# Kernel optimization log

Measured on AMD Instinct MI355X. Metric: run time of the kernel, lower is better.

The kernel has to match this reference:

```python
import jax, jax.numpy as jnp
import numpy as np

B, D, H, T = 8192, 256, 512, 4  # batch, latent dim, hidden units, num IAF transforms


def _made_masks():
    deg_in = np.arange(1, D + 1)                      # input degrees 1..D
    deg_h = 1 + (np.arange(H) % (D - 1))              # hidden degrees in [1, D-1]
    m1 = (deg_h[None, :] >= deg_in[:, None]).astype(np.float32)   # [D, H]
    m2 = (deg_h[None, :] >= deg_h[:, None]).astype(np.float32)    # [H, H]
    mo = (deg_in[None, :] > deg_h[:, None]).astype(np.float32)    # [H, D] strict for outputs
    m3 = np.repeat(mo, 2, axis=1)                     # [H, 2D]: params=2 per dim, interleaved
    return jnp.asarray(m1), jnp.asarray(m2), jnp.asarray(m3)

M1, M2, M3 = _made_masks()


def _made(x, w1, b1, w2, b2, w3, b3):
    h = jax.nn.relu(x @ (w1 * M1) + b1)
    h = jax.nn.relu(h @ (w2 * M2) + b2)
    out = (h @ (w3 * M3) + b3).reshape(x.shape[0], D, 2)
    shift, log_var = out[..., 0], out[..., 1]
    # lstm_flag == False branch of Made.call
    return shift, jnp.tanh(log_var)


def setup_inputs() -> dict:
    key = jax.random.key(0)
    ks = jax.random.split(key, 6)
    s1 = 0.05
    return {
        "mean": jax.random.normal(ks[0], (B, D), jnp.float32),
        "log_var": jax.random.normal(ks[1], (B, D), jnp.float32) * 0.5,
        "eps": jax.random.normal(ks[2], (B, D), jnp.float32),
        "W1": jax.random.normal(ks[3], (T, D, H), jnp.float32) * s1,
        "b1": jnp.zeros((T, H), jnp.float32),
        "W2": jax.random.normal(ks[4], (T, H, H), jnp.float32) * s1,
        "b2": jnp.zeros((T, H), jnp.float32),
        "W3": jax.random.normal(ks[5], (T, H, 2 * D), jnp.float32) * s1,
        "b3": jnp.zeros((T, 2 * D), jnp.float32),
    }


def reference(mean, log_var, eps, W1, b1, W2, b2, W3, b3):
    # Base sample from MultivariateNormalDiag(mean, exp(0.5*log_var))
    x = mean + jnp.exp(0.5 * log_var) * eps
    # Chain([IAF_0, Perm, IAF_1, Perm, ..., IAF_{T-1}, Perm]).forward applies the
    # LAST bijector first: Perm, then Invert(MAF)_{T-1}, ..., down to IAF_0.
    # Invert(MAF).forward == MAF.inverse: a single parallel MADE pass.
    for i in reversed(range(T)):
        x = x[..., ::-1]  # Permute(reversed(range(D)))
        shift, log_scale = _made(x, W1[i], b1[i], W2[i], b2[i], W3[i], b3[i])
        x = (x - shift) * jnp.exp(-log_scale)
    return x
```

## Files before the change

kernel.cpp:

```cpp
#include <hip/hip_runtime.h>


typedef _Float16 f16;
typedef __attribute__((ext_vector_type(8))) _Float16 f16x8;
typedef __attribute__((ext_vector_type(4))) float f32x4;

#define NB 8192
#define ND 256
#define NH 512
#define NT 4
#define XSTR 260

#define W1F_OFF 0
#define W2F_OFF (NT*NH*ND)
#define W3F_OFF (W2F_OFF + NT*NH*NH)
#define WS_ELEMS (W3F_OFF + NT*NH*NH)

__device__ __forceinline__ int h_orig(int j) {
  if (j < 3) return j == 0 ? 0 : (j == 1 ? 255 : 510);
  if (j < 6) return j == 3 ? 1 : (j == 4 ? 256 : 511);
  int d = j >> 1;
  return (j & 1) ? (d + 254) : (d - 1);
}
__device__ __forceinline__ int h_deg(int j) {
  return (j < 3) ? 1 : (j < 6) ? 2 : (j >> 1);
}

__global__ void prep_weights(const float* __restrict__ W1,
                             const float* __restrict__ W2,
                             const float* __restrict__ W3,
                             f16* __restrict__ ws)
{
  int idx = blockIdx.x * blockDim.x + threadIdx.x;
  if (idx >= WS_ELEMS) return;
  float v;
  if (idx < W2F_OFF) {
    int t = idx >> 17, r = idx & ((1 << 17) - 1);
    int e = r & 7, lane = (r >> 3) & 63, ks = (r >> 9) & 7, tile = r >> 12;
    int j = tile * 16 + (lane & 15);
    int k = ks * 32 + (lane >> 4) * 8 + e;
    v = (k <= h_deg(j) - 1) ? W1[t * (ND * NH) + k * NH + h_orig(j)] : 0.f;
  } else if (idx < W3F_OFF) {
    int q = idx - W2F_OFF;
    int t = q >> 18, r = q & ((1 << 18) - 1);
    int e = r & 7, lane = (r >> 3) & 63, ks = (r >> 9) & 15, tile = r >> 13;
    int j = tile * 16 + (lane & 15);
    int k = ks * 32 + (lane >> 4) * 8 + e;
    v = (h_deg(k) <= h_deg(j)) ? W2[t * (NH * NH) + h_orig(k) * NH + h_orig(j)] : 0.f;
  } else {
    int q = idx - W3F_OFF;
    int t = q >> 18, r = q & ((1 << 18) - 1);
    int e = r & 7, lane = (r >> 3) & 63, ks = (r >> 9) & 15, tile = r >> 13;
    int n = tile * 16 + (lane & 15);
    int k = ks * 32 + (lane >> 4) * 8 + e;
    v = (h_deg(k) <= (n >> 1)) ? W3[t * (NH * 2 * ND) + h_orig(k) * (2 * ND) + n] : 0.f;
  }
  ws[idx] = (f16)v;
}

template<int SSTRB>
__device__ __forceinline__ void gemm_pair(const f16* srcA,
                                          const f16* __restrict__ wtA,
                                          const f16* __restrict__ wtB,
                                          int nc, int lrow, int lk8,
                                          f32x4 &accA0, f32x4 &accA1,
                                          f32x4 &accB0, f32x4 &accB1)
{
  const f32x4 z = {0.f, 0.f, 0.f, 0.f};
  accA0 = z; accA1 = z; accB0 = z; accB1 = z;

  f16x8 cA0 = *(const f16x8*)(wtA);
  f16x8 cA1 = *(const f16x8*)(wtA + 512);
  f16x8 cB0 = *(const f16x8*)(wtB);
  f16x8 cB1 = *(const f16x8*)(wtB + 512);

  for (int c = 0; ; ++c) {
    f16x8 nA0, nA1, nB0, nB1;
    const bool more = (c + 1 < nc);
    if (more) {
      const f16* pA = wtA + (c + 1) * 1024;
      const f16* pB = wtB + (c + 1) * 1024;
      nA0 = *(const f16x8*)(pA);
      nA1 = *(const f16x8*)(pA + 512);
      nB0 = *(const f16x8*)(pB);
      nB1 = *(const f16x8*)(pB + 512);
    }
    #pragma unroll
    for (int u = 0; u < 2; ++u) {
      int ks = c * 2 + u;
      int kb = (ks * 32 + lk8 * 8) * 2;
      int off0 = lrow * SSTRB + kb;
      f16x8 a0 = *(const f16x8*)((const char*)srcA + (off0 ^ ((lrow & 7) << 4)));
      int row1 = 16 + lrow;
      int off1 = row1 * SSTRB + kb;
      f16x8 a1 = *(const f16x8*)((const char*)srcA + (off1 ^ ((row1 & 7) << 4)));
      f16x8 bA = u ? cA1 : cA0;
      f16x8 bB = u ? cB1 : cB0;
      accA0 = __builtin_amdgcn_mfma_f32_16x16x32_f16(a0, bA, accA0, 0, 0, 0);
      accA1 = __builtin_amdgcn_mfma_f32_16x16x32_f16(a1, bA, accA1, 0, 0, 0);
      accB0 = __builtin_amdgcn_mfma_f32_16x16x32_f16(a0, bB, accB0, 0, 0, 0);
      accB1 = __builtin_amdgcn_mfma_f32_16x16x32_f16(a1, bB, accB1, 0, 0, 0);
    }
    if (!more) break;
    cA0 = nA0; cA1 = nA1; cB0 = nB0; cB1 = nB1;
  }
}

__device__ __forceinline__ void epi_relu_tile(f32x4 a0, f32x4 a1,
                                              const float* __restrict__ bias_t,
                                              f16* dst, int np, int lrow, int lk8)
{
  const bool ev = (lrow & 1) == 0;
  int n = np + lrow;
  float bv = bias_t[h_orig(n)];
  #pragma unroll
  for (int j = 0; j < 4; ++j) {
    float v0 = fmaxf(a0[j] + bv, 0.f);
    float v1 = fmaxf(a1[j] + bv, 0.f);
    float p0 = __shfl_xor(v0, 1);
    float p1 = __shfl_xor(v1, 1);
    float lo = ev ? v0 : p1;
    float hi = ev ? p0 : v1;
    int m = (ev ? 0 : 16) + lk8 * 4 + j;
    int nw = n & ~1;
    unsigned int w = (unsigned int)__builtin_bit_cast(unsigned short, (f16)lo)
                   | ((unsigned int)__builtin_bit_cast(unsigned short, (f16)hi) << 16);
    int off = m * 1024 + nw * 2;
    *(unsigned int*)((char*)dst + (off ^ ((m & 7) << 4))) = w;
  }
}

__global__ __launch_bounds__(1024, 4) void iaf_main(
    const float* __restrict__ mean, const float* __restrict__ logv,
    const float* __restrict__ eps,
    const float* __restrict__ b1, const float* __restrict__ b2,
    const float* __restrict__ b3,
    const f16* __restrict__ ws, float* __restrict__ out)
{
  __shared__ float xbuf[32][XSTR];
  __shared__ __align__(16) f16 buf0[32 * 512];
  __shared__ __align__(16) f16 buf1[32 * 512];

  const int tid = threadIdx.x;
  const int wid = tid >> 6;
  const int lane = tid & 63;
  const int lrow = lane & 15;
  const int lk8 = lane >> 4;
  const int row0 = blockIdx.x * 32;

  const int tA = 2 * wid, tB = 2 * wid + 1;
  const int npA = tA * 16, npB = tB * 16;
  const int nc1 = wid / 4 + 1;
  const int nc23 = wid / 2 + 1;

  {
    int m = tid >> 5;
    int c0 = (tid & 31) * 8;
    const int g = (row0 + m) * ND + c0;
    #pragma unroll
    for (int i = 0; i < 8; i += 4) {
      f32x4 mu = *(const f32x4*)(mean + g + i);
      f32x4 lv = *(const f32x4*)(logv + g + i);
      f32x4 ep = *(const f32x4*)(eps + g + i);
      f32x4 x;
      #pragma unroll
      for (int q = 0; q < 4; ++q) x[q] = mu[q] + __expf(0.5f * lv[q]) * ep[q];
      *(f32x4*)(&xbuf[m][c0 + i]) = x;
    }
  }
  __syncthreads();

  for (int t = NT - 1; t >= 0; --t) {
    {
      int m = tid >> 5;
      int k0 = (tid & 31) * 8;
      f32x4 lo = *(const f32x4*)(&xbuf[m][248 - k0]);
      f32x4 hi = *(const f32x4*)(&xbuf[m][252 - k0]);
      f16x8 pk;
      pk[0] = (f16)hi[3]; pk[1] = (f16)hi[2]; pk[2] = (f16)hi[1]; pk[3] = (f16)hi[0];
      pk[4] = (f16)lo[3]; pk[5] = (f16)lo[2]; pk[6] = (f16)lo[1]; pk[7] = (f16)lo[0];
      int off = m * 512 + k0 * 2;
      *(f16x8*)((char*)buf0 + (off ^ ((m & 7) << 4))) = pk;
    }
    __syncthreads();

    f32x4 aA0, aA1, aB0, aB1;

    {
      const f16* w1b = ws + W1F_OFF + t * (NH * ND);
      gemm_pair<512>(buf0,
                     w1b + (tA * 8 * 64 + lane) * 8,
                     w1b + (tB * 8 * 64 + lane) * 8,
                     nc1, lrow, lk8, aA0, aA1, aB0, aB1);
      epi_relu_tile(aA0, aA1, b1 + t * NH, buf1, npA, lrow, lk8);
      epi_relu_tile(aB0, aB1, b1 + t * NH, buf1, npB, lrow, lk8);
    }
    __syncthreads();

    {
      const f16* w2b = ws + W2F_OFF + t * (NH * NH);
      gemm_pair<1024>(buf1,
                      w2b + (tA * 16 * 64 + lane) * 8,
                      w2b + (tB * 16 * 64 + lane) * 8,
                      nc23, lrow, lk8, aA0, aA1, aB0, aB1);
      epi_relu_tile(aA0, aA1, b2 + t * NH, buf0, npA, lrow, lk8);
      epi_relu_tile(aB0, aB1, b2 + t * NH, buf0, npB, lrow, lk8);
    }
    __syncthreads();

    {
      const f16* w3b = ws + W3F_OFF + t * (NH * NH);
      gemm_pair<1024>(buf0,
                      w3b + (tA * 16 * 64 + lane) * 8,
                      w3b + (tB * 16 * 64 + lane) * 8,
                      nc23, lrow, lk8, aA0, aA1, aB0, aB1);

      const bool ev = (lrow & 1) == 0;
      const float* b3t = b3 + t * (2 * ND);
      float xnA[2][4], xnB[2][4];
      #pragma unroll
      for (int pt = 0; pt < 2; ++pt) {
        f32x4 o_0 = pt ? aB0 : aA0;
        f32x4 o_1 = pt ? aB1 : aA1;
        float (*xn)[4] = pt ? xnB : xnA;
        int n = (pt ? npB : npA) + lrow;
        float bv = b3t[n];
        #pragma unroll
        for (int j = 0; j < 4; ++j) {
          float o0 = o_0[j] + bv;
          float o1 = o_1[j] + bv;
          float po0 = __shfl_xor(o0, 1);
          float po1 = __shfl_xor(o1, 1);
          if (ev) {
            int d = n >> 1;
            float xc0 = xbuf[lk8 * 4 + j][255 - d];
            float e0 = __expf(2.f * po0);
            float t0 = 1.f - 2.f / (e0 + 1.f);
            xn[0][j] = (xc0 - o0) * __expf(-t0);
            float xc1 = xbuf[16 + lk8 * 4 + j][255 - d];
            float e1 = __expf(2.f * po1);
            float t1 = 1.f - 2.f / (e1 + 1.f);
            xn[1][j] = (xc1 - o1) * __expf(-t1);
          }
        }
      }
      __syncthreads();
      if (ev) {
        int dA = (npA + lrow) >> 1;
        int dB = (npB + lrow) >> 1;
        #pragma unroll
        for (int j = 0; j < 4; ++j) {
          xbuf[lk8 * 4 + j][dA]      = xnA[0][j];
          xbuf[16 + lk8 * 4 + j][dA] = xnA[1][j];
          xbuf[lk8 * 4 + j][dB]      = xnB[0][j];
          xbuf[16 + lk8 * 4 + j][dB] = xnB[1][j];
        }
      }
      __syncthreads();
    }
  }

  {
    int m = tid >> 5;
    int c0 = (tid & 31) * 8;
    float* op = out + (row0 + m) * ND + c0;
    #pragma unroll
    for (int i = 0; i < 8; i += 4)
      *(f32x4*)(op + i) = *(const f32x4*)(&xbuf[m][c0 + i]);
  }
}

extern "C" void kernel_launch(void* const* d_in, const int* in_sizes, int n_in,
                              void* d_out, int out_size, void* d_ws, size_t ws_size,
                              hipStream_t stream) {
  const float* mean = (const float*)d_in[0];
  const float* logv = (const float*)d_in[1];
  const float* eps  = (const float*)d_in[2];
  const float* W1   = (const float*)d_in[3];
  const float* b1   = (const float*)d_in[4];
  const float* W2   = (const float*)d_in[5];
  const float* b2   = (const float*)d_in[6];
  const float* W3   = (const float*)d_in[7];
  const float* b3   = (const float*)d_in[8];
  f16* ws = (f16*)d_ws;

  prep_weights<<<(WS_ELEMS + 255) / 256, 256, 0, stream>>>(W1, W2, W3, ws);
  iaf_main<<<NB / 32, 1024, 0, stream>>>(mean, logv, eps, b1, b2, b3, ws,
                                         (float*)d_out);
}
```

Before: 78.94 us.

## Triple-buffer weight fragments and prefetch next GEMM's weights across stage boundaries

```diff
diff --git a/kernel.cpp b/kernel.cpp
--- a/kernel.cpp
+++ b/kernel.cpp
@@ -58,54 +58,6 @@
   ws[idx] = (f16)v;
 }
 
-template<int SSTRB>
-__device__ __forceinline__ void gemm_pair(const f16* srcA,
-                                          const f16* __restrict__ wtA,
-                                          const f16* __restrict__ wtB,
-                                          int nc, int lrow, int lk8,
-                                          f32x4 &accA0, f32x4 &accA1,
-                                          f32x4 &accB0, f32x4 &accB1)
-{
-  const f32x4 z = {0.f, 0.f, 0.f, 0.f};
-  accA0 = z; accA1 = z; accB0 = z; accB1 = z;
-
-  f16x8 cA0 = *(const f16x8*)(wtA);
-  f16x8 cA1 = *(const f16x8*)(wtA + 512);
-  f16x8 cB0 = *(const f16x8*)(wtB);
-  f16x8 cB1 = *(const f16x8*)(wtB + 512);
-
-  for (int c = 0; ; ++c) {
-    f16x8 nA0, nA1, nB0, nB1;
-    const bool more = (c + 1 < nc);
-    if (more) {
-      const f16* pA = wtA + (c + 1) * 1024;
-      const f16* pB = wtB + (c + 1) * 1024;
-      nA0 = *(const f16x8*)(pA);
-      nA1 = *(const f16x8*)(pA + 512);
-      nB0 = *(const f16x8*)(pB);
-      nB1 = *(const f16x8*)(pB + 512);
-    }
-    #pragma unroll
-    for (int u = 0; u < 2; ++u) {
-      int ks = c * 2 + u;
-      int kb = (ks * 32 + lk8 * 8) * 2;
-      int off0 = lrow * SSTRB + kb;
-      f16x8 a0 = *(const f16x8*)((const char*)srcA + (off0 ^ ((lrow & 7) << 4)));
-      int row1 = 16 + lrow;
-      int off1 = row1 * SSTRB + kb;
-      f16x8 a1 = *(const f16x8*)((const char*)srcA + (off1 ^ ((row1 & 7) << 4)));
-      f16x8 bA = u ? cA1 : cA0;
-      f16x8 bB = u ? cB1 : cB0;
-      accA0 = __builtin_amdgcn_mfma_f32_16x16x32_f16(a0, bA, accA0, 0, 0, 0);
-      accA1 = __builtin_amdgcn_mfma_f32_16x16x32_f16(a1, bA, accA1, 0, 0, 0);
-      accB0 = __builtin_amdgcn_mfma_f32_16x16x32_f16(a0, bB, accB0, 0, 0, 0);
-      accB1 = __builtin_amdgcn_mfma_f32_16x16x32_f16(a1, bB, accB1, 0, 0, 0);
-    }
-    if (!more) break;
-    cA0 = nA0; cA1 = nA1; cB0 = nB0; cB1 = nB1;
-  }
-}
-
 __device__ __forceinline__ void epi_relu_tile(f32x4 a0, f32x4 a1,
                                               const float* __restrict__ bias_t,
                                               f16* dst, int np, int lrow, int lk8)
@@ -130,6 +82,60 @@
   }
 }
 
+#define MFMA16 __builtin_amdgcn_mfma_f32_16x16x32_f16
+
+#define LOAD_SLOT(S, cidx) do {                          \
+    const f16* _pA = _wtA + (cidx) * 1024;               \
+    const f16* _pB = _wtB + (cidx) * 1024;               \
+    S##a0 = *(const f16x8*)(_pA);                        \
+    S##a1 = *(const f16x8*)(_pA + 512);                  \
+    S##b0 = *(const f16x8*)(_pB);                        \
+    S##b1 = *(const f16x8*)(_pB + 512);                  \
+  } while (0)
+
+#define USE_SLOT(S, srcA, SST, cc) do {                                   \
+    int _kb = 128 * (cc) + lk8 * 16;                                      \
+    int _r1 = 16 + lrow;                                                  \
+    int _oA0 = (lrow * (SST) + _kb) ^ ((lrow & 7) << 4);                  \
+    int _oA1 = (_r1 * (SST) + _kb) ^ ((_r1 & 7) << 4);                    \
+    int _oB0 = (lrow * (SST) + _kb + 64) ^ ((lrow & 7) << 4);             \
+    int _oB1 = (_r1 * (SST) + _kb + 64) ^ ((_r1 & 7) << 4);               \
+    f16x8 _x00 = *(const f16x8*)((const char*)(srcA) + _oA0);             \
+    f16x8 _x10 = *(const f16x8*)((const char*)(srcA) + _oA1);             \
+    f16x8 _x01 = *(const f16x8*)((const char*)(srcA) + _oB0);             \
+    f16x8 _x11 = *(const f16x8*)((const char*)(srcA) + _oB1);             \
+    aA0 = MFMA16(_x00, S##a0, aA0, 0, 0, 0);                              \
+    aA1 = MFMA16(_x10, S##a0, aA1, 0, 0, 0);                              \
+    aB0 = MFMA16(_x00, S##b0, aB0, 0, 0, 0);                              \
+    aB1 = MFMA16(_x10, S##b0, aB1, 0, 0, 0);                              \
+    aA0 = MFMA16(_x01, S##a1, aA0, 0, 0, 0);                              \
+    aA1 = MFMA16(_x11, S##a1, aA1, 0, 0, 0);                              \
+    aB0 = MFMA16(_x01, S##b1, aB0, 0, 0, 0);                              \
+    aB1 = MFMA16(_x11, S##b1, aB1, 0, 0, 0);                              \
+  } while (0)
+
+#define B_PROLOGUE(pA, pB) do {                          \
+    _wtA = (pA); _wtB = (pB);                            \
+    LOAD_SLOT(q0, 0); LOAD_SLOT(q1, 1); LOAD_SLOT(q2, 2);\
+  } while (0)
+
+#define ZERO_ACCS do { aA0 = z4; aA1 = z4; aB0 = z4; aB1 = z4; } while (0)
+
+#define GEMM_LOOP(srcA, SST, ncv) do {                   \
+    int _c = 0;                                          \
+    for (;;) {                                           \
+      USE_SLOT(q0, srcA, SST, _c);                       \
+      if (_c + 3 < (ncv)) LOAD_SLOT(q0, _c + 3);         \
+      if (++_c == (ncv)) break;                          \
+      USE_SLOT(q1, srcA, SST, _c);                       \
+      if (_c + 3 < (ncv)) LOAD_SLOT(q1, _c + 3);         \
+      if (++_c == (ncv)) break;                          \
+      USE_SLOT(q2, srcA, SST, _c);                       \
+      if (_c + 3 < (ncv)) LOAD_SLOT(q2, _c + 3);         \
+      if (++_c == (ncv)) break;                          \
+    }                                                    \
+  } while (0)
+
 __global__ __launch_bounds__(1024, 4) void iaf_main(
     const float* __restrict__ mean, const float* __restrict__ logv,
     const float* __restrict__ eps,
@@ -152,6 +158,16 @@
   const int npA = tA * 16, npB = tB * 16;
   const int nc1 = wid / 4 + 1;
   const int nc23 = wid / 2 + 1;
+
+  const f32x4 z4 = {0.f, 0.f, 0.f, 0.f};
+  f32x4 aA0, aA1, aB0, aB1;
+  const f16 *_wtA, *_wtB;
+  f16x8 q0a0, q0a1, q0b0, q0b1;
+  f16x8 q1a0, q1a1, q1b0, q1b1;
+  f16x8 q2a0, q2a1, q2b0, q2b1;
+
+  const int o1A = tA * 4096 + lane * 8, o1B = tB * 4096 + lane * 8;
+  const int o2A = tA * 8192 + lane * 8, o2B = tB * 8192 + lane * 8;
 
   {
     int m = tid >> 5;
@@ -168,6 +184,9 @@
       *(f32x4*)(&xbuf[m][c0 + i]) = x;
     }
   }
+
+  B_PROLOGUE(ws + W1F_OFF + 3 * (NH * ND) + o1A,
+             ws + W1F_OFF + 3 * (NH * ND) + o1B);
   __syncthreads();
 
   for (int t = NT - 1; t >= 0; --t) {
@@ -184,37 +203,30 @@
     }
     __syncthreads();
 
-    f32x4 aA0, aA1, aB0, aB1;
-
+    ZERO_ACCS;
+    GEMM_LOOP(buf0, 512, nc1);
+    B_PROLOGUE(ws + W2F_OFF + t * (NH * NH) + o2A,
+               ws + W2F_OFF + t * (NH * NH) + o2B);
+    epi_relu_tile(aA0, aA1, b1 + t * NH, buf1, npA, lrow, lk8);
+    epi_relu_tile(aB0, aB1, b1 + t * NH, buf1, npB, lrow, lk8);
+    __syncthreads();
+
+    ZERO_ACCS;
+    GEMM_LOOP(buf1, 1024, nc23);
+    B_PROLOGUE(ws + W3F_OFF + t * (NH * NH) + o2A,
+               ws + W3F_OFF + t * (NH * NH) + o2B);
+    epi_relu_tile(aA0, aA1, b2 + t * NH, buf0, npA, lrow, lk8);
+    epi_relu_tile(aB0, aB1, b2 + t * NH, buf0, npB, lrow, lk8);
+    __syncthreads();
+
+    ZERO_ACCS;
+    GEMM_LOOP(buf0, 1024, nc23);
     {
-      const f16* w1b = ws + W1F_OFF + t * (NH * ND);
-      gemm_pair<512>(buf0,
-                     w1b + (tA * 8 * 64 + lane) * 8,
-                     w1b + (tB * 8 * 64 + lane) * 8,
-                     nc1, lrow, lk8, aA0, aA1, aB0, aB1);
-      epi_relu_tile(aA0, aA1, b1 + t * NH, buf1, npA, lrow, lk8);
-      epi_relu_tile(aB0, aB1, b1 + t * NH, buf1, npB, lrow, lk8);
+      const int tn = (t > 0) ? (t - 1) : 0;
+      B_PROLOGUE(ws + W1F_OFF + tn * (NH * ND) + o1A,
+                 ws + W1F_OFF + tn * (NH * ND) + o1B);
     }
-    __syncthreads();
-
     {
-      const f16* w2b = ws + W2F_OFF + t * (NH * NH);
-      gemm_pair<1024>(buf1,
-                      w2b + (tA * 16 * 64 + lane) * 8,
-                      w2b + (tB * 16 * 64 + lane) * 8,
-                      nc23, lrow, lk8, aA0, aA1, aB0, aB1);
-      epi_relu_tile(aA0, aA1, b2 + t * NH, buf0, npA, lrow, lk8);
-      epi_relu_tile(aB0, aB1, b2 + t * NH, buf0, npB, lrow, lk8);
-    }
-    __syncthreads();
-
-    {
-      const f16* w3b = ws + W3F_OFF + t * (NH * NH);
-      gemm_pair<1024>(buf0,
-                      w3b + (tA * 16 * 64 + lane) * 8,
-                      w3b + (tB * 16 * 64 + lane) * 8,
-                      nc23, lrow, lk8, aA0, aA1, aB0, aB1);
-
       const bool ev = (lrow & 1) == 0;
       const float* b3t = b3 + t * (2 * ND);
       float xnA[2][4], xnB[2][4];
```

After: 76.85 us. 1.03x faster.

## Balance triangular MADE GEMM work by pairing small and large column tiles per wave

Applied to the files above, without the earlier changes.

```diff
diff --git a/kernel.cpp b/kernel.cpp
--- a/kernel.cpp
+++ b/kernel.cpp
@@ -58,51 +58,77 @@
   ws[idx] = (f16)v;
 }
 
+#define MFMA16 __builtin_amdgcn_mfma_f32_16x16x32_f16
+
 template<int SSTRB>
-__device__ __forceinline__ void gemm_pair(const f16* srcA,
-                                          const f16* __restrict__ wtA,
-                                          const f16* __restrict__ wtB,
-                                          int nc, int lrow, int lk8,
-                                          f32x4 &accA0, f32x4 &accA1,
-                                          f32x4 &accB0, f32x4 &accB1)
+__device__ __forceinline__ void gemm_hybrid(const f16* srcA,
+                                            const f16* __restrict__ wtS,
+                                            const f16* __restrict__ wtB,
+                                            int ncS, int ncB,
+                                            int lrow, int lk8,
+                                            f32x4 &aS0, f32x4 &aS1,
+                                            f32x4 &aB0, f32x4 &aB1)
 {
   const f32x4 z = {0.f, 0.f, 0.f, 0.f};
-  accA0 = z; accA1 = z; accB0 = z; accB1 = z;
-
-  f16x8 cA0 = *(const f16x8*)(wtA);
-  f16x8 cA1 = *(const f16x8*)(wtA + 512);
+  aS0 = z; aS1 = z; aB0 = z; aB1 = z;
+  const int r1 = 16 + lrow;
+  const int swz0 = (lrow & 7) << 4;
+  const int swz1 = (r1 & 7) << 4;
+
+  f16x8 cS0 = *(const f16x8*)(wtS);
+  f16x8 cS1 = *(const f16x8*)(wtS + 512);
   f16x8 cB0 = *(const f16x8*)(wtB);
   f16x8 cB1 = *(const f16x8*)(wtB + 512);
-
   for (int c = 0; ; ++c) {
-    f16x8 nA0, nA1, nB0, nB1;
-    const bool more = (c + 1 < nc);
+    f16x8 nS0, nS1, nB0, nB1;
+    const bool more = (c + 1 < ncS);
     if (more) {
-      const f16* pA = wtA + (c + 1) * 1024;
+      const f16* pS = wtS + (c + 1) * 1024;
       const f16* pB = wtB + (c + 1) * 1024;
-      nA0 = *(const f16x8*)(pA);
-      nA1 = *(const f16x8*)(pA + 512);
+      nS0 = *(const f16x8*)(pS);
+      nS1 = *(const f16x8*)(pS + 512);
       nB0 = *(const f16x8*)(pB);
       nB1 = *(const f16x8*)(pB + 512);
     }
     #pragma unroll
     for (int u = 0; u < 2; ++u) {
-      int ks = c * 2 + u;
-      int kb = (ks * 32 + lk8 * 8) * 2;
-      int off0 = lrow * SSTRB + kb;
-      f16x8 a0 = *(const f16x8*)((const char*)srcA + (off0 ^ ((lrow & 7) << 4)));
-      int row1 = 16 + lrow;
-      int off1 = row1 * SSTRB + kb;
-      f16x8 a1 = *(const f16x8*)((const char*)srcA + (off1 ^ ((row1 & 7) << 4)));
-      f16x8 bA = u ? cA1 : cA0;
+      int kb = 128 * c + u * 64 + lk8 * 16;
+      f16x8 a0 = *(const f16x8*)((const char*)srcA + ((lrow * SSTRB + kb) ^ swz0));
+      f16x8 a1 = *(const f16x8*)((const char*)srcA + ((r1 * SSTRB + kb) ^ swz1));
+      f16x8 bS = u ? cS1 : cS0;
       f16x8 bB = u ? cB1 : cB0;
-      accA0 = __builtin_amdgcn_mfma_f32_16x16x32_f16(a0, bA, accA0, 0, 0, 0);
-      accA1 = __builtin_amdgcn_mfma_f32_16x16x32_f16(a1, bA, accA1, 0, 0, 0);
-      accB0 = __builtin_amdgcn_mfma_f32_16x16x32_f16(a0, bB, accB0, 0, 0, 0);
-      accB1 = __builtin_amdgcn_mfma_f32_16x16x32_f16(a1, bB, accB1, 0, 0, 0);
+      aS0 = MFMA16(a0, bS, aS0, 0, 0, 0);
+      aS1 = MFMA16(a1, bS, aS1, 0, 0, 0);
+      aB0 = MFMA16(a0, bB, aB0, 0, 0, 0);
+      aB1 = MFMA16(a1, bB, aB1, 0, 0, 0);
     }
     if (!more) break;
-    cA0 = nA0; cA1 = nA1; cB0 = nB0; cB1 = nB1;
+    cS0 = nS0; cS1 = nS1; cB0 = nB0; cB1 = nB1;
+  }
+
+  if (ncS < ncB) {
+    f16x8 dB0 = *(const f16x8*)(wtB + ncS * 1024);
+    f16x8 dB1 = *(const f16x8*)(wtB + ncS * 1024 + 512);
+    for (int c = ncS; ; ++c) {
+      f16x8 nB0, nB1;
+      const bool more = (c + 1 < ncB);
+      if (more) {
+        const f16* pB = wtB + (c + 1) * 1024;
+        nB0 = *(const f16x8*)(pB);
+        nB1 = *(const f16x8*)(pB + 512);
+      }
+      #pragma unroll
+      for (int u = 0; u < 2; ++u) {
+        int kb = 128 * c + u * 64 + lk8 * 16;
+        f16x8 a0 = *(const f16x8*)((const char*)srcA + ((lrow * SSTRB + kb) ^ swz0));
+        f16x8 a1 = *(const f16x8*)((const char*)srcA + ((r1 * SSTRB + kb) ^ swz1));
+        f16x8 bB = u ? dB1 : dB0;
+        aB0 = MFMA16(a0, bB, aB0, 0, 0, 0);
+        aB1 = MFMA16(a1, bB, aB1, 0, 0, 0);
+      }
+      if (!more) break;
+      dB0 = nB0; dB1 = nB1;
+    }
   }
 }
 
@@ -148,10 +174,10 @@
   const int lk8 = lane >> 4;
   const int row0 = blockIdx.x * 32;
 
-  const int tA = 2 * wid, tB = 2 * wid + 1;
-  const int npA = tA * 16, npB = tB * 16;
-  const int nc1 = wid / 4 + 1;
-  const int nc23 = wid / 2 + 1;
+  const int tS = wid, tB = 31 - wid;
+  const int npS = tS * 16, npB = tB * 16;
+  const int nc1S = tS / 8 + 1, nc1B = tB / 8 + 1;
+  const int nc23S = tS / 4 + 1, nc23B = tB / 4 + 1;
 
   {
     int m = tid >> 5;
@@ -184,46 +210,46 @@
     }
     __syncthreads();
 
-    f32x4 aA0, aA1, aB0, aB1;
+    f32x4 aS0, aS1, aB0, aB1;
 
     {
       const f16* w1b = ws + W1F_OFF + t * (NH * ND);
-      gemm_pair<512>(buf0,
-                     w1b + (tA * 8 * 64 + lane) * 8,
-                     w1b + (tB * 8 * 64 + lane) * 8,
-                     nc1, lrow, lk8, aA0, aA1, aB0, aB1);
-      epi_relu_tile(aA0, aA1, b1 + t * NH, buf1, npA, lrow, lk8);
+      gemm_hybrid<512>(buf0,
+                       w1b + tS * 4096 + lane * 8,
+                       w1b + tB * 4096 + lane * 8,
+                       nc1S, nc1B, lrow, lk8, aS0, aS1, aB0, aB1);
+      epi_relu_tile(aS0, aS1, b1 + t * NH, buf1, npS, lrow, lk8);
       epi_relu_tile(aB0, aB1, b1 + t * NH, buf1, npB, lrow, lk8);
     }
     __syncthreads();
 
     {
       const f16* w2b = ws + W2F_OFF + t * (NH * NH);
-      gemm_pair<1024>(buf1,
-                      w2b + (tA * 16 * 64 + lane) * 8,
-                      w2b + (tB * 16 * 64 + lane) * 8,
-                      nc23, lrow, lk8, aA0, aA1, aB0, aB1);
-      epi_relu_tile(aA0, aA1, b2 + t * NH, buf0, npA, lrow, lk8);
+      gemm_hybrid<1024>(buf1,
+                        w2b + tS * 8192 + lane * 8,
+                        w2b + tB * 8192 + lane * 8,
+                        nc23S, nc23B, lrow, lk8, aS0, aS1, aB0, aB1);
+      epi_relu_tile(aS0, aS1, b2 + t * NH, buf0, npS, lrow, lk8);
       epi_relu_tile(aB0, aB1, b2 + t * NH, buf0, npB, lrow, lk8);
     }
     __syncthreads();
 
     {
       const f16* w3b = ws + W3F_OFF + t * (NH * NH);
-      gemm_pair<1024>(buf0,
-                      w3b + (tA * 16 * 64 + lane) * 8,
-                      w3b + (tB * 16 * 64 + lane) * 8,
-                      nc23, lrow, lk8, aA0, aA1, aB0, aB1);
+      gemm_hybrid<1024>(buf0,
+                        w3b + tS * 8192 + lane * 8,
+                        w3b + tB * 8192 + lane * 8,
+                        nc23S, nc23B, lrow, lk8, aS0, aS1, aB0, aB1);
 
       const bool ev = (lrow & 1) == 0;
       const float* b3t = b3 + t * (2 * ND);
-      float xnA[2][4], xnB[2][4];
+      float xnS[2][4], xnB[2][4];
       #pragma unroll
       for (int pt = 0; pt < 2; ++pt) {
-        f32x4 o_0 = pt ? aB0 : aA0;
-        f32x4 o_1 = pt ? aB1 : aA1;
-        float (*xn)[4] = pt ? xnB : xnA;
-        int n = (pt ? npB : npA) + lrow;
+        f32x4 o_0 = pt ? aB0 : aS0;
+        f32x4 o_1 = pt ? aB1 : aS1;
+        float (*xn)[4] = pt ? xnB : xnS;
+        int n = (pt ? npB : npS) + lrow;
         float bv = b3t[n];
         #pragma unroll
         for (int j = 0; j < 4; ++j) {
@@ -246,12 +272,12 @@
       }
       __syncthreads();
       if (ev) {
-        int dA = (npA + lrow) >> 1;
+        int dS = (npS + lrow) >> 1;
         int dB = (npB + lrow) >> 1;
         #pragma unroll
         for (int j = 0; j < 4; ++j) {
-          xbuf[lk8 * 4 + j][dA]      = xnA[0][j];
-          xbuf[16 + lk8 * 4 + j][dA] = xnA[1][j];
+          xbuf[lk8 * 4 + j][dS]      = xnS[0][j];
+          xbuf[16 + lk8 * 4 + j][dS] = xnS[1][j];
           xbuf[lk8 * 4 + j][dB]      = xnB[0][j];
           xbuf[16 + lk8 * 4 + j][dB] = xnB[1][j];
         }
```

New measurement: 78.77 us. No clear change (-0.2%).
